# Optimization experiments

Measured on AMD Instinct MI355X. Metric: run time of the kernel, lower is better.

## Reference

```python
import jax, jax.numpy as jnp
import numpy as np

N = 50000          # num nodes
DEG = 16           # fixed degree (uniform CSR)
E = N * DEG        # num edges
R = 8              # num relations
IN = 128
HID = 128
OUT = 40
BN_EPS = 1e-5


def setup_inputs() -> dict:
    key = jax.random.key(0)
    k = jax.random.split(key, 5)
    x = jax.random.normal(k[0], (N, IN), jnp.float32)
    # glorot-ish init for per-relation weights
    W1 = jax.random.normal(k[1], (R, IN, HID), jnp.float32) * (2.0 / (IN + HID)) ** 0.5
    W2 = jax.random.normal(k[2], (R, HID, OUT), jnp.float32) * (2.0 / (HID + OUT)) ** 0.5
    ptr = jnp.arange(N + 1, dtype=jnp.int32) * DEG            # CSR row offsets
    idx = jax.random.randint(k[3], (E,), 0, N, jnp.int32)     # neighbor (src) ids
    edge_types = jax.random.randint(k[4], (E,), 0, R, jnp.int32)
    return {
        "x": x, "W1": W1, "W2": W2,
        "bn_gamma": jnp.ones((HID,), jnp.float32),
        "bn_beta": jnp.zeros((HID,), jnp.float32),
        "bn_mean": jnp.zeros((HID,), jnp.float32),
        "bn_var": jnp.ones((HID,), jnp.float32),
        "ptr": ptr, "idx": idx, "edge_types": edge_types,
    }


def _rgcn_layer(h, W, ptr, idx, edge_types):
    # RGCNOP: out[i] = sum_{e in [ptr[i],ptr[i+1])} x[idx[e]] @ W[etype[e]]
    # Efficient form: transform every node by every relation once, then gather
    # the (src, etype) pair per edge and scatter-add into destinations.
    xr = jnp.einsum('nd,rdh->nrh', h, W)             # [N, R, H]
    msgs = xr[idx, edge_types]                       # [E, H] irregular gather
    deg = ptr[1:] - ptr[:-1]                         # [N]
    dst = jnp.repeat(jnp.arange(ptr.shape[0] - 1, dtype=jnp.int32), deg,
                     total_repeat_length=idx.shape[0])
    agg = jax.ops.segment_sum(msgs, dst, num_segments=ptr.shape[0] - 1)
    return agg / deg[:, None].astype(agg.dtype)      # degree normalization


def reference(x, W1, W2, bn_gamma, bn_beta, bn_mean, bn_var, ptr, idx, edge_types):
    h = _rgcn_layer(x, W1, ptr, idx, edge_types)
    # BatchNorm1d in eval mode (history_size=0, dropout inactive)
    h = (h - bn_mean) * jax.lax.rsqrt(bn_var + BN_EPS) * bn_gamma + bn_beta
    h = jax.nn.relu(h)
    h = _rgcn_layer(h, W2, ptr, idx, edge_types)
    return jax.nn.log_softmax(h, axis=-1)
```

## Files before the change

kernel.cpp:

```cpp
#include <hip/hip_runtime.h>
#include <math.h>

typedef __attribute__((ext_vector_type(8))) short bf16x8;
typedef __attribute__((ext_vector_type(4))) float f32x4;

constexpr int kN   = 50000;
constexpr int kR   = 8;
constexpr int kIn  = 128;
constexpr int kHid = 128;
constexpr int kOut = 40;
constexpr int kNT  = 16;
constexpr int kLds = 1032;
constexpr float kBnEps = 1e-5f;

__device__ inline ushort f2bf(float x) {
    uint u = __float_as_uint(x);
    u += 0x7FFFu + ((u >> 16) & 1u);
    return (ushort)(u >> 16);
}
__device__ inline float bf2f(ushort s) { return __uint_as_float(((uint)s) << 16); }

__global__ void cast_x(const float* __restrict__ x, ushort* __restrict__ xb)
{
    const size_t i = ((size_t)blockIdx.x * 256 + threadIdx.x) * 8;
    const float4 v0 = *(const float4*)&x[i];
    const float4 v1 = *(const float4*)&x[i + 4];
    *(ushort4*)&xb[i]     = make_ushort4(f2bf(v0.x), f2bf(v0.y), f2bf(v0.z), f2bf(v0.w));
    *(ushort4*)&xb[i + 4] = make_ushort4(f2bf(v1.x), f2bf(v1.y), f2bf(v1.z), f2bf(v1.w));
}

__global__ void pack_w(const float* __restrict__ W, ushort* __restrict__ hi, int N)
{
    const int lane = threadIdx.x;
    const int kt = blockIdx.x & 31;
    const int nt = blockIdx.x >> 5;
    const int n  = nt * 16 + (lane & 15);
    const int q  = lane >> 4;
    ushort hv[8];
    #pragma unroll
    for (int j = 0; j < 8; ++j) {
        const int k = kt * 32 + q * 8 + j;
        hv[j] = f2bf((n < N) ? W[(size_t)k * N + n] : 0.f);
    }
    const size_t o = ((size_t)blockIdx.x * 64 + lane) * 8;
    *(ushort4*)&hi[o]     = make_ushort4(hv[0], hv[1], hv[2], hv[3]);
    *(ushort4*)&hi[o + 4] = make_ushort4(hv[4], hv[5], hv[6], hv[7]);
}

#define ACCUM_ET(ET, VX, VY)                                   \
    if      ((ET) == 0) { a0.x += (VX); a0.y += (VY); }        \
    else if ((ET) == 1) { a1.x += (VX); a1.y += (VY); }        \
    else if ((ET) == 2) { a2.x += (VX); a2.y += (VY); }        \
    else if ((ET) == 3) { a3.x += (VX); a3.y += (VY); }        \
    else if ((ET) == 4) { a4.x += (VX); a4.y += (VY); }        \
    else if ((ET) == 5) { a5.x += (VX); a5.y += (VY); }        \
    else if ((ET) == 6) { a6.x += (VX); a6.y += (VY); }        \
    else                { a7.x += (VX); a7.y += (VY); }

#define GATHER(BV, SRC) \
    const ushort2 BV = *(const ushort2*)&feat[(size_t)(SRC) * 128 + d2];

#define ACCUM_EDGE(J, BV) \
    { const int et = __builtin_amdgcn_readlane(ve, J); ACCUM_ET(et, bf2f(BV.x), bf2f(BV.y)) }

#define STORE_AGG(RR, AV) \
    *(ushort2*)&aggHi[n][(RR) * 128 + d2] = make_ushort2(f2bf(AV.x), f2bf(AV.y));

__device__ __forceinline__ void phaseA_bf16(const ushort* __restrict__ feat,
                                            const int* __restrict__ ptr,
                                            const int* __restrict__ idx,
                                            const int* __restrict__ etype,
                                            int base, ushort (*aggHi)[kLds])
{
    const int lane = threadIdx.x & 63;
    const int wid  = threadIdx.x >> 6;
    const int d2   = lane * 2;

    #pragma unroll
    for (int t = 0; t < 2; ++t) {
        const int n    = wid * 2 + t;
        const int node = base + n;
        const int p0   = ptr[node];
        const int deg  = ptr[node + 1] - p0;

        float2 a0 = {0.f,0.f}, a1 = {0.f,0.f}, a2 = {0.f,0.f}, a3 = {0.f,0.f};
        float2 a4 = {0.f,0.f}, a5 = {0.f,0.f}, a6 = {0.f,0.f}, a7 = {0.f,0.f};

        if (deg == 16) {
            const int vi = idx[p0 + (lane & 15)];
            const int ve = etype[p0 + (lane & 15)];
            const int s0  = __builtin_amdgcn_readlane(vi, 0);
            const int s1  = __builtin_amdgcn_readlane(vi, 1);
            const int s2  = __builtin_amdgcn_readlane(vi, 2);
            const int s3  = __builtin_amdgcn_readlane(vi, 3);
            const int s4  = __builtin_amdgcn_readlane(vi, 4);
            const int s5  = __builtin_amdgcn_readlane(vi, 5);
            const int s6  = __builtin_amdgcn_readlane(vi, 6);
            const int s7  = __builtin_amdgcn_readlane(vi, 7);
            const int s8  = __builtin_amdgcn_readlane(vi, 8);
            const int s9  = __builtin_amdgcn_readlane(vi, 9);
            const int s10 = __builtin_amdgcn_readlane(vi, 10);
            const int s11 = __builtin_amdgcn_readlane(vi, 11);
            const int s12 = __builtin_amdgcn_readlane(vi, 12);
            const int s13 = __builtin_amdgcn_readlane(vi, 13);
            const int s14 = __builtin_amdgcn_readlane(vi, 14);
            const int s15 = __builtin_amdgcn_readlane(vi, 15);
            GATHER(b0,  s0)  GATHER(b1,  s1)  GATHER(b2,  s2)  GATHER(b3,  s3)
            GATHER(b4,  s4)  GATHER(b5,  s5)  GATHER(b6,  s6)  GATHER(b7,  s7)
            GATHER(b8,  s8)  GATHER(b9,  s9)  GATHER(b10, s10) GATHER(b11, s11)
            GATHER(b12, s12) GATHER(b13, s13) GATHER(b14, s14) GATHER(b15, s15)
            ACCUM_EDGE(0,  b0)  ACCUM_EDGE(1,  b1)  ACCUM_EDGE(2,  b2)  ACCUM_EDGE(3,  b3)
            ACCUM_EDGE(4,  b4)  ACCUM_EDGE(5,  b5)  ACCUM_EDGE(6,  b6)  ACCUM_EDGE(7,  b7)
            ACCUM_EDGE(8,  b8)  ACCUM_EDGE(9,  b9)  ACCUM_EDGE(10, b10) ACCUM_EDGE(11, b11)
            ACCUM_EDGE(12, b12) ACCUM_EDGE(13, b13) ACCUM_EDGE(14, b14) ACCUM_EDGE(15, b15)
        } else {
            for (int e = p0; e < p0 + deg; ++e) {
                const int src = __builtin_amdgcn_readfirstlane(idx[e]);
                const int et  = __builtin_amdgcn_readfirstlane(etype[e]);
                const ushort2 u = *(const ushort2*)&feat[(size_t)src * 128 + d2];
                ACCUM_ET(et, bf2f(u.x), bf2f(u.y))
            }
        }
        STORE_AGG(0, a0) STORE_AGG(1, a1) STORE_AGG(2, a2) STORE_AGG(3, a3)
        STORE_AGG(4, a4) STORE_AGG(5, a5) STORE_AGG(6, a6) STORE_AGG(7, a7)
    }
}

__global__ __launch_bounds__(512, 4)
void rgcn_layer1(const ushort* __restrict__ xb,
                 const ushort* __restrict__ W1hi,
                 const float* __restrict__ gamma, const float* __restrict__ beta,
                 const float* __restrict__ mean,  const float* __restrict__ var,
                 const int* __restrict__ ptr, const int* __restrict__ idx,
                 const int* __restrict__ etype,
                 ushort* __restrict__ h1b)
{
    __shared__ ushort aggHi[kNT][kLds];
    const int tid  = threadIdx.x;
    const int base = blockIdx.x * kNT;

    phaseA_bf16(xb, ptr, idx, etype, base, aggHi);
    __syncthreads();

    const int lane = tid & 63;
    const int wid  = tid >> 6;
    const int m    = lane & 15;
    const int q    = lane >> 4;

    const bf16x8* Bh = (const bf16x8*)W1hi + (size_t)wid * 32 * 64 + lane;
    f32x4 acc = {0.f, 0.f, 0.f, 0.f};

    #pragma unroll 4
    for (int kt = 0; kt < 32; ++kt) {
        const bf16x8 ah = *(const bf16x8*)&aggHi[m][kt * 32 + q * 8];
        const bf16x8 bh = Bh[(size_t)kt * 64];
        acc = __builtin_amdgcn_mfma_f32_16x16x32_bf16(ah, bh, acc, 0, 0, 0);
    }

    const int c = wid * 16 + m;
    const float g  = gamma[c] * rsqrtf(var[c] + kBnEps);
    const float mu = mean[c];
    const float bt = beta[c];
    #pragma unroll
    for (int i = 0; i < 4; ++i) {
        const int node = base + q * 4 + i;
        const float invdeg = 1.0f / (float)(ptr[node + 1] - ptr[node]);
        float v = (acc[i] * invdeg - mu) * g + bt;
        v = fmaxf(v, 0.f);
        h1b[(size_t)node * kHid + c] = f2bf(v);
    }
}

__global__ __launch_bounds__(512, 4)
void rgcn_layer2(const ushort* __restrict__ h1b,
                 const ushort* __restrict__ W2hi,
                 const int* __restrict__ ptr, const int* __restrict__ idx,
                 const int* __restrict__ etype,
                 float* __restrict__ out)
{
    __shared__ ushort aggHi[kNT][kLds];
    __shared__ float logits[kNT][48];
    const int tid  = threadIdx.x;
    const int base = blockIdx.x * kNT;

    phaseA_bf16(h1b, ptr, idx, etype, base, aggHi);
    __syncthreads();

    const int lane = tid & 63;
    const int wid  = tid >> 6;
    const int m    = lane & 15;
    const int q    = lane >> 4;

    if (wid < 3) {
        const bf16x8* Bh = (const bf16x8*)W2hi + (size_t)wid * 32 * 64 + lane;
        f32x4 acc = {0.f, 0.f, 0.f, 0.f};
        #pragma unroll 4
        for (int kt = 0; kt < 32; ++kt) {
            const bf16x8 ah = *(const bf16x8*)&aggHi[m][kt * 32 + q * 8];
            const bf16x8 bh = Bh[(size_t)kt * 64];
            acc = __builtin_amdgcn_mfma_f32_16x16x32_bf16(ah, bh, acc, 0, 0, 0);
        }
        const int n = wid * 16 + m;
        if (n < kOut) {
            #pragma unroll
            for (int i = 0; i < 4; ++i) {
                const int node = base + q * 4 + i;
                const float invdeg = 1.0f / (float)(ptr[node + 1] - ptr[node]);
                logits[q * 4 + i][n] = acc[i] * invdeg;
            }
        }
    }
    __syncthreads();

    #pragma unroll
    for (int i = 0; i < 2; ++i) {
        const int nrow = wid * 2 + i;
        const int node = base + nrow;
        const float v = (lane < kOut) ? logits[nrow][lane] : -INFINITY;
        float mx = v;
        #pragma unroll
        for (int off = 32; off > 0; off >>= 1)
            mx = fmaxf(mx, __shfl_xor(mx, off, 64));
        float s = (lane < kOut) ? __expf(v - mx) : 0.f;
        #pragma unroll
        for (int off = 32; off > 0; off >>= 1)
            s += __shfl_xor(s, off, 64);
        if (lane < kOut)
            out[(size_t)node * kOut + lane] = v - mx - __logf(s);
    }
}

extern "C" void kernel_launch(void* const* d_in, const int* in_sizes, int n_in,
                              void* d_out, int out_size, void* d_ws, size_t ws_size,
                              hipStream_t stream)
{
    const float* x     = (const float*)d_in[0];
    const float* W1    = (const float*)d_in[1];
    const float* W2    = (const float*)d_in[2];
    const float* gamma = (const float*)d_in[3];
    const float* beta  = (const float*)d_in[4];
    const float* mean  = (const float*)d_in[5];
    const float* var   = (const float*)d_in[6];
    const int*   ptr   = (const int*)d_in[7];
    const int*   idx   = (const int*)d_in[8];
    const int*   et    = (const int*)d_in[9];
    float*       out   = (float*)d_out;

    char* ws = (char*)d_ws;
    ushort* h1b  = (ushort*)ws;
    ushort* xb   = (ushort*)(ws + 12800000);
    ushort* W1hi = (ushort*)(ws + 25600000);
    ushort* W2hi = (ushort*)(ws + 25600000 + 262144);

    cast_x<<<dim3(3125), dim3(256), 0, stream>>>(x, xb);
    pack_w<<<dim3(8 * 32), dim3(64), 0, stream>>>(W1, W1hi, kHid);
    pack_w<<<dim3(3 * 32), dim3(64), 0, stream>>>(W2, W2hi, kOut);

    dim3 grid(kN / kNT), block(512);
    rgcn_layer1<<<grid, block, 0, stream>>>(xb, W1hi, gamma, beta, mean, var,
                                            ptr, idx, et, h1b);
    rgcn_layer2<<<grid, block, 0, stream>>>(h1b, W2hi, ptr, idx, et, out);
}
```

Baseline: 200.6 us.

## Merge prep kernels, scalar-load edge metadata, split MFMA accumulators

```diff
diff --git a/kernel.cpp b/kernel.cpp
--- a/kernel.cpp
+++ b/kernel.cpp
@@ -1,8 +1,10 @@
 #include <hip/hip_runtime.h>
 #include <math.h>
 
-typedef __attribute__((ext_vector_type(8))) short bf16x8;
-typedef __attribute__((ext_vector_type(4))) float f32x4;
+typedef __attribute__((ext_vector_type(8)))  short bf16x8;
+typedef __attribute__((ext_vector_type(4)))  float f32x4;
+typedef __attribute__((ext_vector_type(2)))  float f32x2;
+typedef __attribute__((ext_vector_type(16))) int   i32x16;
 
 constexpr int kN   = 50000;
 constexpr int kR   = 8;
@@ -18,22 +20,22 @@
     u += 0x7FFFu + ((u >> 16) & 1u);
     return (ushort)(u >> 16);
 }
-__device__ inline float bf2f(ushort s) { return __uint_as_float(((uint)s) << 16); }
-
-__global__ void cast_x(const float* __restrict__ x, ushort* __restrict__ xb)
-{
-    const size_t i = ((size_t)blockIdx.x * 256 + threadIdx.x) * 8;
-    const float4 v0 = *(const float4*)&x[i];
-    const float4 v1 = *(const float4*)&x[i + 4];
-    *(ushort4*)&xb[i]     = make_ushort4(f2bf(v0.x), f2bf(v0.y), f2bf(v0.z), f2bf(v0.w));
-    *(ushort4*)&xb[i + 4] = make_ushort4(f2bf(v1.x), f2bf(v1.y), f2bf(v1.z), f2bf(v1.w));
-}
-
-__global__ void pack_w(const float* __restrict__ W, ushort* __restrict__ hi, int N)
-{
-    const int lane = threadIdx.x;
-    const int kt = blockIdx.x & 31;
-    const int nt = blockIdx.x >> 5;
+
+__device__ __forceinline__ void sload_meta(const int* pi, const int* pt,
+                                           i32x16& vi, i32x16& vt)
+{
+    asm volatile("s_load_dwordx16 %0, %2, 0x0\n\t"
+                 "s_load_dwordx16 %1, %3, 0x0\n\t"
+                 "s_waitcnt lgkmcnt(0)"
+                 : "=s"(vi), "=s"(vt) : "s"(pi), "s"(pt));
+}
+
+__device__ __forceinline__ void pack_unit(const float* __restrict__ W,
+                                          ushort* __restrict__ dst,
+                                          int N, int frag, int lane)
+{
+    const int kt = frag & 31;
+    const int nt = frag >> 5;
     const int n  = nt * 16 + (lane & 15);
     const int q  = lane >> 4;
     ushort hv[8];
@@ -42,29 +44,48 @@
         const int k = kt * 32 + q * 8 + j;
         hv[j] = f2bf((n < N) ? W[(size_t)k * N + n] : 0.f);
     }
-    const size_t o = ((size_t)blockIdx.x * 64 + lane) * 8;
-    *(ushort4*)&hi[o]     = make_ushort4(hv[0], hv[1], hv[2], hv[3]);
-    *(ushort4*)&hi[o + 4] = make_ushort4(hv[4], hv[5], hv[6], hv[7]);
-}
-
-#define ACCUM_ET(ET, VX, VY)                                   \
-    if      ((ET) == 0) { a0.x += (VX); a0.y += (VY); }        \
-    else if ((ET) == 1) { a1.x += (VX); a1.y += (VY); }        \
-    else if ((ET) == 2) { a2.x += (VX); a2.y += (VY); }        \
-    else if ((ET) == 3) { a3.x += (VX); a3.y += (VY); }        \
-    else if ((ET) == 4) { a4.x += (VX); a4.y += (VY); }        \
-    else if ((ET) == 5) { a5.x += (VX); a5.y += (VY); }        \
-    else if ((ET) == 6) { a6.x += (VX); a6.y += (VY); }        \
-    else                { a7.x += (VX); a7.y += (VY); }
-
-#define GATHER(BV, SRC) \
-    const ushort2 BV = *(const ushort2*)&feat[(size_t)(SRC) * 128 + d2];
-
-#define ACCUM_EDGE(J, BV) \
-    { const int et = __builtin_amdgcn_readlane(ve, J); ACCUM_ET(et, bf2f(BV.x), bf2f(BV.y)) }
-
-#define STORE_AGG(RR, AV) \
-    *(ushort2*)&aggHi[n][(RR) * 128 + d2] = make_ushort2(f2bf(AV.x), f2bf(AV.y));
+    const size_t o = ((size_t)frag * 64 + lane) * 8;
+    *(ushort4*)&dst[o]     = make_ushort4(hv[0], hv[1], hv[2], hv[3]);
+    *(ushort4*)&dst[o + 4] = make_ushort4(hv[4], hv[5], hv[6], hv[7]);
+}
+
+__global__ __launch_bounds__(256)
+void prep(const float* __restrict__ x,  ushort* __restrict__ xb,
+          const float* __restrict__ W1, ushort* __restrict__ W1hi,
+          const float* __restrict__ W2, ushort* __restrict__ W2hi)
+{
+    const int b   = blockIdx.x;
+    const int tid = threadIdx.x;
+    if (b < 3125) {
+        const size_t i = ((size_t)b * 256 + tid) * 8;
+        const float4 v0 = *(const float4*)&x[i];
+        const float4 v1 = *(const float4*)&x[i + 4];
+        *(ushort4*)&xb[i]     = make_ushort4(f2bf(v0.x), f2bf(v0.y), f2bf(v0.z), f2bf(v0.w));
+        *(ushort4*)&xb[i + 4] = make_ushort4(f2bf(v1.x), f2bf(v1.y), f2bf(v1.z), f2bf(v1.w));
+    } else if (b < 3125 + 64) {
+        pack_unit(W1, W1hi, kHid, (b - 3125) * 4 + (tid >> 6), tid & 63);
+    } else {
+        const int frag = (b - 3189) * 4 + (tid >> 6);
+        if (frag < 96) pack_unit(W2, W2hi, kOut, frag, tid & 63);
+    }
+}
+
+#define CVT_ACC(T, B) {                                                     \
+    f32x2 v;                                                                \
+    v.x = __uint_as_float((B) << 16);                                       \
+    v.y = __uint_as_float((B) & 0xffff0000u);                               \
+    if      ((T) == 0) a0 += v; else if ((T) == 1) a1 += v;                 \
+    else if ((T) == 2) a2 += v; else if ((T) == 3) a3 += v;                 \
+    else if ((T) == 4) a4 += v; else if ((T) == 5) a5 += v;                 \
+    else if ((T) == 6) a6 += v; else               a7 += v; }
+
+#define GATH(BV, S) \
+    const uint BV = *(const uint*)(feat + (size_t)(S) * 128 + d2);
+
+#define STORE_AGG(RR, AV) {                                                 \
+    const uint px = (__float_as_uint(AV.x) + 0x8000u) >> 16;                \
+    const uint py = (__float_as_uint(AV.y) + 0x8000u) & 0xffff0000u;        \
+    *(uint*)&aggHi[n][(RR) * 128 + d2] = px | py; }
 
 __device__ __forceinline__ void phaseA_bf16(const ushort* __restrict__ feat,
                                             const int* __restrict__ ptr,
@@ -80,45 +101,31 @@
     for (int t = 0; t < 2; ++t) {
         const int n    = wid * 2 + t;
         const int node = base + n;
-        const int p0   = ptr[node];
-        const int deg  = ptr[node + 1] - p0;
-
-        float2 a0 = {0.f,0.f}, a1 = {0.f,0.f}, a2 = {0.f,0.f}, a3 = {0.f,0.f};
-        float2 a4 = {0.f,0.f}, a5 = {0.f,0.f}, a6 = {0.f,0.f}, a7 = {0.f,0.f};
+        const int p0   = __builtin_amdgcn_readfirstlane(ptr[node]);
+        const int deg  = __builtin_amdgcn_readfirstlane(ptr[node + 1]) - p0;
+
+        f32x2 a0 = {0.f,0.f}, a1 = {0.f,0.f}, a2 = {0.f,0.f}, a3 = {0.f,0.f};
+        f32x2 a4 = {0.f,0.f}, a5 = {0.f,0.f}, a6 = {0.f,0.f}, a7 = {0.f,0.f};
 
         if (deg == 16) {
-            const int vi = idx[p0 + (lane & 15)];
-            const int ve = etype[p0 + (lane & 15)];
-            const int s0  = __builtin_amdgcn_readlane(vi, 0);
-            const int s1  = __builtin_amdgcn_readlane(vi, 1);
-            const int s2  = __builtin_amdgcn_readlane(vi, 2);
-            const int s3  = __builtin_amdgcn_readlane(vi, 3);
-            const int s4  = __builtin_amdgcn_readlane(vi, 4);
-            const int s5  = __builtin_amdgcn_readlane(vi, 5);
-            const int s6  = __builtin_amdgcn_readlane(vi, 6);
-            const int s7  = __builtin_amdgcn_readlane(vi, 7);
-            const int s8  = __builtin_amdgcn_readlane(vi, 8);
-            const int s9  = __builtin_amdgcn_readlane(vi, 9);
-            const int s10 = __builtin_amdgcn_readlane(vi, 10);
-            const int s11 = __builtin_amdgcn_readlane(vi, 11);
-            const int s12 = __builtin_amdgcn_readlane(vi, 12);
-            const int s13 = __builtin_amdgcn_readlane(vi, 13);
-            const int s14 = __builtin_amdgcn_readlane(vi, 14);
-            const int s15 = __builtin_amdgcn_readlane(vi, 15);
-            GATHER(b0,  s0)  GATHER(b1,  s1)  GATHER(b2,  s2)  GATHER(b3,  s3)
-            GATHER(b4,  s4)  GATHER(b5,  s5)  GATHER(b6,  s6)  GATHER(b7,  s7)
-            GATHER(b8,  s8)  GATHER(b9,  s9)  GATHER(b10, s10) GATHER(b11, s11)
-            GATHER(b12, s12) GATHER(b13, s13) GATHER(b14, s14) GATHER(b15, s15)
-            ACCUM_EDGE(0,  b0)  ACCUM_EDGE(1,  b1)  ACCUM_EDGE(2,  b2)  ACCUM_EDGE(3,  b3)
-            ACCUM_EDGE(4,  b4)  ACCUM_EDGE(5,  b5)  ACCUM_EDGE(6,  b6)  ACCUM_EDGE(7,  b7)
-            ACCUM_EDGE(8,  b8)  ACCUM_EDGE(9,  b9)  ACCUM_EDGE(10, b10) ACCUM_EDGE(11, b11)
-            ACCUM_EDGE(12, b12) ACCUM_EDGE(13, b13) ACCUM_EDGE(14, b14) ACCUM_EDGE(15, b15)
+            i32x16 vi, vt;
+            sload_meta(idx + p0, etype + p0, vi, vt);
+            GATH(b0,  vi[0])  GATH(b1,  vi[1])  GATH(b2,  vi[2])  GATH(b3,  vi[3])
+            GATH(b4,  vi[4])  GATH(b5,  vi[5])  GATH(b6,  vi[6])  GATH(b7,  vi[7])
+            GATH(b8,  vi[8])  GATH(b9,  vi[9])  GATH(b10, vi[10]) GATH(b11, vi[11])
+            GATH(b12, vi[12]) GATH(b13, vi[13]) GATH(b14, vi[14]) GATH(b15, vi[15])
+            CVT_ACC(vt[0],  b0)  CVT_ACC(vt[1],  b1)  CVT_ACC(vt[2],  b2)
+            CVT_ACC(vt[3],  b3)  CVT_ACC(vt[4],  b4)  CVT_ACC(vt[5],  b5)
+            CVT_ACC(vt[6],  b6)  CVT_ACC(vt[7],  b7)  CVT_ACC(vt[8],  b8)
+            CVT_ACC(vt[9],  b9)  CVT_ACC(vt[10], b10) CVT_ACC(vt[11], b11)
+            CVT_ACC(vt[12], b12) CVT_ACC(vt[13], b13) CVT_ACC(vt[14], b14)
+            CVT_ACC(vt[15], b15)
         } else {
             for (int e = p0; e < p0 + deg; ++e) {
                 const int src = __builtin_amdgcn_readfirstlane(idx[e]);
                 const int et  = __builtin_amdgcn_readfirstlane(etype[e]);
-                const ushort2 u = *(const ushort2*)&feat[(size_t)src * 128 + d2];
-                ACCUM_ET(et, bf2f(u.x), bf2f(u.y))
+                const uint u  = *(const uint*)(feat + (size_t)src * 128 + d2);
+                CVT_ACC(et, u)
             }
         }
         STORE_AGG(0, a0) STORE_AGG(1, a1) STORE_AGG(2, a2) STORE_AGG(3, a3)
@@ -148,14 +155,19 @@
     const int q    = lane >> 4;
 
     const bf16x8* Bh = (const bf16x8*)W1hi + (size_t)wid * 32 * 64 + lane;
-    f32x4 acc = {0.f, 0.f, 0.f, 0.f};
+    f32x4 accA = {0.f, 0.f, 0.f, 0.f};
+    f32x4 accB = {0.f, 0.f, 0.f, 0.f};
 
     #pragma unroll 4
-    for (int kt = 0; kt < 32; ++kt) {
-        const bf16x8 ah = *(const bf16x8*)&aggHi[m][kt * 32 + q * 8];
-        const bf16x8 bh = Bh[(size_t)kt * 64];
-        acc = __builtin_amdgcn_mfma_f32_16x16x32_bf16(ah, bh, acc, 0, 0, 0);
-    }
+    for (int kt = 0; kt < 32; kt += 2) {
+        const bf16x8 ah0 = *(const bf16x8*)&aggHi[m][kt * 32 + q * 8];
+        const bf16x8 bh0 = Bh[(size_t)kt * 64];
+        const bf16x8 ah1 = *(const bf16x8*)&aggHi[m][(kt + 1) * 32 + q * 8];
+        const bf16x8 bh1 = Bh[(size_t)(kt + 1) * 64];
+        accA = __builtin_amdgcn_mfma_f32_16x16x32_bf16(ah0, bh0, accA, 0, 0, 0);
+        accB = __builtin_amdgcn_mfma_f32_16x16x32_bf16(ah1, bh1, accB, 0, 0, 0);
+    }
+    const f32x4 acc = accA + accB;
 
     const int c = wid * 16 + m;
     const float g  = gamma[c] * rsqrtf(var[c] + kBnEps);
@@ -167,7 +179,7 @@
         const float invdeg = 1.0f / (float)(ptr[node + 1] - ptr[node]);
         float v = (acc[i] * invdeg - mu) * g + bt;
         v = fmaxf(v, 0.f);
-        h1b[(size_t)node * kHid + c] = f2bf(v);
+        h1b[(size_t)node * kHid + c] = (ushort)((__float_as_uint(v) + 0x8000u) >> 16);
     }
 }
 
@@ -193,13 +205,18 @@
 
     if (wid < 3) {
         const bf16x8* Bh = (const bf16x8*)W2hi + (size_t)wid * 32 * 64 + lane;
-        f32x4 acc = {0.f, 0.f, 0.f, 0.f};
+        f32x4 accA = {0.f, 0.f, 0.f, 0.f};
+        f32x4 accB = {0.f, 0.f, 0.f, 0.f};
         #pragma unroll 4
-        for (int kt = 0; kt < 32; ++kt) {
-            const bf16x8 ah = *(const bf16x8*)&aggHi[m][kt * 32 + q * 8];
-            const bf16x8 bh = Bh[(size_t)kt * 64];
-            acc = __builtin_amdgcn_mfma_f32_16x16x32_bf16(ah, bh, acc, 0, 0, 0);
+        for (int kt = 0; kt < 32; kt += 2) {
+            const bf16x8 ah0 = *(const bf16x8*)&aggHi[m][kt * 32 + q * 8];
+            const bf16x8 bh0 = Bh[(size_t)kt * 64];
+            const bf16x8 ah1 = *(const bf16x8*)&aggHi[m][(kt + 1) * 32 + q * 8];
+            const bf16x8 bh1 = Bh[(size_t)(kt + 1) * 64];
+            accA = __builtin_amdgcn_mfma_f32_16x16x32_bf16(ah0, bh0, accA, 0, 0, 0);
+            accB = __builtin_amdgcn_mfma_f32_16x16x32_bf16(ah1, bh1, accB, 0, 0, 0);
         }
+        const f32x4 acc = accA + accB;
         const int n = wid * 16 + m;
         if (n < kOut) {
             #pragma unroll
@@ -252,9 +269,7 @@
     ushort* W1hi = (ushort*)(ws + 25600000);
     ushort* W2hi = (ushort*)(ws + 25600000 + 262144);
 
-    cast_x<<<dim3(3125), dim3(256), 0, stream>>>(x, xb);
-    pack_w<<<dim3(8 * 32), dim3(64), 0, stream>>>(W1, W1hi, kHid);
-    pack_w<<<dim3(3 * 32), dim3(64), 0, stream>>>(W2, W2hi, kOut);
+    prep<<<dim3(3125 + 64 + 24), dim3(256), 0, stream>>>(x, xb, W1, W1hi, W2, W2hi);
 
     dim3 grid(kN / kNT), block(512);
     rgcn_layer1<<<grid, block, 0, stream>>>(xb, W1hi, gamma, beta, mean, var,
```

Measured after the change: 209.0 us. 4.2% more time.

## Fuse prep kernels, software-pipeline MFMA loads, simplify bf16 conversions

Applied to the files above, without the earlier changes.

```diff
diff --git a/kernel.cpp b/kernel.cpp
--- a/kernel.cpp
+++ b/kernel.cpp
@@ -18,22 +18,13 @@
     u += 0x7FFFu + ((u >> 16) & 1u);
     return (ushort)(u >> 16);
 }
-__device__ inline float bf2f(ushort s) { return __uint_as_float(((uint)s) << 16); }
-
-__global__ void cast_x(const float* __restrict__ x, ushort* __restrict__ xb)
-{
-    const size_t i = ((size_t)blockIdx.x * 256 + threadIdx.x) * 8;
-    const float4 v0 = *(const float4*)&x[i];
-    const float4 v1 = *(const float4*)&x[i + 4];
-    *(ushort4*)&xb[i]     = make_ushort4(f2bf(v0.x), f2bf(v0.y), f2bf(v0.z), f2bf(v0.w));
-    *(ushort4*)&xb[i + 4] = make_ushort4(f2bf(v1.x), f2bf(v1.y), f2bf(v1.z), f2bf(v1.w));
-}
-
-__global__ void pack_w(const float* __restrict__ W, ushort* __restrict__ hi, int N)
-{
-    const int lane = threadIdx.x;
-    const int kt = blockIdx.x & 31;
-    const int nt = blockIdx.x >> 5;
+
+__device__ __forceinline__ void pack_unit(const float* __restrict__ W,
+                                          ushort* __restrict__ dst,
+                                          int N, int frag, int lane)
+{
+    const int kt = frag & 31;
+    const int nt = frag >> 5;
     const int n  = nt * 16 + (lane & 15);
     const int q  = lane >> 4;
     ushort hv[8];
@@ -42,29 +33,54 @@
         const int k = kt * 32 + q * 8 + j;
         hv[j] = f2bf((n < N) ? W[(size_t)k * N + n] : 0.f);
     }
-    const size_t o = ((size_t)blockIdx.x * 64 + lane) * 8;
-    *(ushort4*)&hi[o]     = make_ushort4(hv[0], hv[1], hv[2], hv[3]);
-    *(ushort4*)&hi[o + 4] = make_ushort4(hv[4], hv[5], hv[6], hv[7]);
-}
-
-#define ACCUM_ET(ET, VX, VY)                                   \
-    if      ((ET) == 0) { a0.x += (VX); a0.y += (VY); }        \
-    else if ((ET) == 1) { a1.x += (VX); a1.y += (VY); }        \
-    else if ((ET) == 2) { a2.x += (VX); a2.y += (VY); }        \
-    else if ((ET) == 3) { a3.x += (VX); a3.y += (VY); }        \
-    else if ((ET) == 4) { a4.x += (VX); a4.y += (VY); }        \
-    else if ((ET) == 5) { a5.x += (VX); a5.y += (VY); }        \
-    else if ((ET) == 6) { a6.x += (VX); a6.y += (VY); }        \
-    else                { a7.x += (VX); a7.y += (VY); }
-
-#define GATHER(BV, SRC) \
-    const ushort2 BV = *(const ushort2*)&feat[(size_t)(SRC) * 128 + d2];
+    const size_t o = ((size_t)frag * 64 + lane) * 8;
+    *(ushort4*)&dst[o]     = make_ushort4(hv[0], hv[1], hv[2], hv[3]);
+    *(ushort4*)&dst[o + 4] = make_ushort4(hv[4], hv[5], hv[6], hv[7]);
+}
+
+__global__ __launch_bounds__(256)
+void prep(const float* __restrict__ x,  ushort* __restrict__ xb,
+          const float* __restrict__ W1, ushort* __restrict__ W1hi,
+          const float* __restrict__ W2, ushort* __restrict__ W2hi)
+{
+    const int b   = blockIdx.x;
+    const int tid = threadIdx.x;
+    if (b < 3125) {
+        const size_t i = ((size_t)b * 256 + tid) * 8;
+        const float4 v0 = *(const float4*)&x[i];
+        const float4 v1 = *(const float4*)&x[i + 4];
+        *(ushort4*)&xb[i]     = make_ushort4(f2bf(v0.x), f2bf(v0.y), f2bf(v0.z), f2bf(v0.w));
+        *(ushort4*)&xb[i + 4] = make_ushort4(f2bf(v1.x), f2bf(v1.y), f2bf(v1.z), f2bf(v1.w));
+    } else if (b < 3125 + 64) {
+        pack_unit(W1, W1hi, kHid, (b - 3125) * 4 + (tid >> 6), tid & 63);
+    } else {
+        const int frag = (b - 3189) * 4 + (tid >> 6);
+        if (frag < 96) pack_unit(W2, W2hi, kOut, frag, tid & 63);
+    }
+}
+
+#define ACC_ET(ET, BV) {                                                    \
+    const float vx = __uint_as_float((BV) << 16);                           \
+    const float vy = __uint_as_float((BV) & 0xffff0000u);                   \
+    if      ((ET) == 0) { a0.x += vx; a0.y += vy; }                         \
+    else if ((ET) == 1) { a1.x += vx; a1.y += vy; }                         \
+    else if ((ET) == 2) { a2.x += vx; a2.y += vy; }                         \
+    else if ((ET) == 3) { a3.x += vx; a3.y += vy; }                         \
+    else if ((ET) == 4) { a4.x += vx; a4.y += vy; }                         \
+    else if ((ET) == 5) { a5.x += vx; a5.y += vy; }                         \
+    else if ((ET) == 6) { a6.x += vx; a6.y += vy; }                         \
+    else                { a7.x += vx; a7.y += vy; } }
+
+#define GATH(BV, S) \
+    const uint BV = *(const uint*)(feat + (size_t)(S) * 128 + d2);
 
 #define ACCUM_EDGE(J, BV) \
-    { const int et = __builtin_amdgcn_readlane(ve, J); ACCUM_ET(et, bf2f(BV.x), bf2f(BV.y)) }
-
-#define STORE_AGG(RR, AV) \
-    *(ushort2*)&aggHi[n][(RR) * 128 + d2] = make_ushort2(f2bf(AV.x), f2bf(AV.y));
+    { const int et_ = __builtin_amdgcn_readlane(ve, J); ACC_ET(et_, BV) }
+
+#define STORE_AGG(RR, AV) {                                                 \
+    const uint px = (__float_as_uint(AV.x) + 0x8000u) >> 16;                \
+    const uint py = (__float_as_uint(AV.y) + 0x8000u) & 0xffff0000u;        \
+    *(uint*)&aggHi[n][(RR) * 128 + d2] = px | py; }
 
 __device__ __forceinline__ void phaseA_bf16(const ushort* __restrict__ feat,
                                             const int* __restrict__ ptr,
@@ -78,7 +94,7 @@
 
     #pragma unroll
     for (int t = 0; t < 2; ++t) {
-        const int n    = wid * 2 + t;
+        const int n    = wid + t * 8;
         const int node = base + n;
         const int p0   = ptr[node];
         const int deg  = ptr[node + 1] - p0;
@@ -105,20 +121,22 @@
             const int s13 = __builtin_amdgcn_readlane(vi, 13);
             const int s14 = __builtin_amdgcn_readlane(vi, 14);
             const int s15 = __builtin_amdgcn_readlane(vi, 15);
-            GATHER(b0,  s0)  GATHER(b1,  s1)  GATHER(b2,  s2)  GATHER(b3,  s3)
-            GATHER(b4,  s4)  GATHER(b5,  s5)  GATHER(b6,  s6)  GATHER(b7,  s7)
-            GATHER(b8,  s8)  GATHER(b9,  s9)  GATHER(b10, s10) GATHER(b11, s11)
-            GATHER(b12, s12) GATHER(b13, s13) GATHER(b14, s14) GATHER(b15, s15)
-            ACCUM_EDGE(0,  b0)  ACCUM_EDGE(1,  b1)  ACCUM_EDGE(2,  b2)  ACCUM_EDGE(3,  b3)
-            ACCUM_EDGE(4,  b4)  ACCUM_EDGE(5,  b5)  ACCUM_EDGE(6,  b6)  ACCUM_EDGE(7,  b7)
-            ACCUM_EDGE(8,  b8)  ACCUM_EDGE(9,  b9)  ACCUM_EDGE(10, b10) ACCUM_EDGE(11, b11)
-            ACCUM_EDGE(12, b12) ACCUM_EDGE(13, b13) ACCUM_EDGE(14, b14) ACCUM_EDGE(15, b15)
+            GATH(b0,  s0)  GATH(b1,  s1)  GATH(b2,  s2)  GATH(b3,  s3)
+            GATH(b4,  s4)  GATH(b5,  s5)  GATH(b6,  s6)  GATH(b7,  s7)
+            GATH(b8,  s8)  GATH(b9,  s9)  GATH(b10, s10) GATH(b11, s11)
+            GATH(b12, s12) GATH(b13, s13) GATH(b14, s14) GATH(b15, s15)
+            ACCUM_EDGE(0,  b0)  ACCUM_EDGE(1,  b1)  ACCUM_EDGE(2,  b2)
+            ACCUM_EDGE(3,  b3)  ACCUM_EDGE(4,  b4)  ACCUM_EDGE(5,  b5)
+            ACCUM_EDGE(6,  b6)  ACCUM_EDGE(7,  b7)  ACCUM_EDGE(8,  b8)
+            ACCUM_EDGE(9,  b9)  ACCUM_EDGE(10, b10) ACCUM_EDGE(11, b11)
+            ACCUM_EDGE(12, b12) ACCUM_EDGE(13, b13) ACCUM_EDGE(14, b14)
+            ACCUM_EDGE(15, b15)
         } else {
             for (int e = p0; e < p0 + deg; ++e) {
                 const int src = __builtin_amdgcn_readfirstlane(idx[e]);
-                const int et  = __builtin_amdgcn_readfirstlane(etype[e]);
-                const ushort2 u = *(const ushort2*)&feat[(size_t)src * 128 + d2];
-                ACCUM_ET(et, bf2f(u.x), bf2f(u.y))
+                const int et_ = __builtin_amdgcn_readfirstlane(etype[e]);
+                const uint u  = *(const uint*)(feat + (size_t)src * 128 + d2);
+                ACC_ET(et_, u)
             }
         }
         STORE_AGG(0, a0) STORE_AGG(1, a1) STORE_AGG(2, a2) STORE_AGG(3, a3)
@@ -148,13 +166,19 @@
     const int q    = lane >> 4;
 
     const bf16x8* Bh = (const bf16x8*)W1hi + (size_t)wid * 32 * 64 + lane;
+    bf16x8 bc = Bh[0];
+    bf16x8 bn = Bh[64];
+    bf16x8 ac = *(const bf16x8*)&aggHi[m][q * 8];
     f32x4 acc = {0.f, 0.f, 0.f, 0.f};
 
-    #pragma unroll 4
+    #pragma unroll
     for (int kt = 0; kt < 32; ++kt) {
-        const bf16x8 ah = *(const bf16x8*)&aggHi[m][kt * 32 + q * 8];
-        const bf16x8 bh = Bh[(size_t)kt * 64];
-        acc = __builtin_amdgcn_mfma_f32_16x16x32_bf16(ah, bh, acc, 0, 0, 0);
+        const int ktb = (kt + 2 < 32) ? kt + 2 : 0;
+        const int kta = (kt + 1 < 32) ? kt + 1 : 0;
+        const bf16x8 bf_ = Bh[(size_t)ktb * 64];
+        const bf16x8 af_ = *(const bf16x8*)&aggHi[m][kta * 32 + q * 8];
+        acc = __builtin_amdgcn_mfma_f32_16x16x32_bf16(ac, bc, acc, 0, 0, 0);
+        ac = af_; bc = bn; bn = bf_;
     }
 
     const int c = wid * 16 + m;
@@ -167,7 +191,7 @@
         const float invdeg = 1.0f / (float)(ptr[node + 1] - ptr[node]);
         float v = (acc[i] * invdeg - mu) * g + bt;
         v = fmaxf(v, 0.f);
-        h1b[(size_t)node * kHid + c] = f2bf(v);
+        h1b[(size_t)node * kHid + c] = (ushort)((__float_as_uint(v) + 0x8000u) >> 16);
     }
 }
 
@@ -193,12 +217,18 @@
 
     if (wid < 3) {
         const bf16x8* Bh = (const bf16x8*)W2hi + (size_t)wid * 32 * 64 + lane;
+        bf16x8 bc = Bh[0];
+        bf16x8 bn = Bh[64];
+        bf16x8 ac = *(const bf16x8*)&aggHi[m][q * 8];
         f32x4 acc = {0.f, 0.f, 0.f, 0.f};
-        #pragma unroll 4
+        #pragma unroll
         for (int kt = 0; kt < 32; ++kt) {
-            const bf16x8 ah = *(const bf16x8*)&aggHi[m][kt * 32 + q * 8];
-            const bf16x8 bh = Bh[(size_t)kt * 64];
-            acc = __builtin_amdgcn_mfma_f32_16x16x32_bf16(ah, bh, acc, 0, 0, 0);
+            const int ktb = (kt + 2 < 32) ? kt + 2 : 0;
+            const int kta = (kt + 1 < 32) ? kt + 1 : 0;
+            const bf16x8 bf_ = Bh[(size_t)ktb * 64];
+            const bf16x8 af_ = *(const bf16x8*)&aggHi[m][kta * 32 + q * 8];
+            acc = __builtin_amdgcn_mfma_f32_16x16x32_bf16(ac, bc, acc, 0, 0, 0);
+            ac = af_; bc = bn; bn = bf_;
         }
         const int n = wid * 16 + m;
         if (n < kOut) {
@@ -252,9 +282,7 @@
     ushort* W1hi = (ushort*)(ws + 25600000);
     ushort* W2hi = (ushort*)(ws + 25600000 + 262144);
 
-    cast_x<<<dim3(3125), dim3(256), 0, stream>>>(x, xb);
-    pack_w<<<dim3(8 * 32), dim3(64), 0, stream>>>(W1, W1hi, kHid);
-    pack_w<<<dim3(3 * 32), dim3(64), 0, stream>>>(W2, W2hi, kOut);
+    prep<<<dim3(3125 + 64 + 24), dim3(256), 0, stream>>>(x, xb, W1, W1hi, W2, W2hi);
 
     dim3 grid(kN / kNT), block(512);
     rgcn_layer1<<<grid, block, 0, stream>>>(xb, W1hi, gamma, beta, mean, var,
```

Result: no change. 203.7 us (+1.6%).
